# Kernel tuning notes

Hardware: AMD Instinct MI355X
Metric: run time of the kernel (lower is better)

Reference implementation:

```python
import jax, jax.numpy as jnp
import numpy as np

N = 50000   # nodes
E = 600000  # edges (avg degree 12)
D = 128     # embedding dim (hardcoded in original: np.zeros(128))
P = 5       # propagation iterations (self.p)


def setup_inputs() -> dict:
    key = jax.random.key(0)
    ks = jax.random.split(key, 10)
    x = jax.random.normal(ks[0], (N, D), jnp.float32)
    g = jax.random.normal(ks[1], (D,), jnp.float32)
    dist = jax.random.uniform(ks[2], (E,), jnp.float32)
    w1 = jax.random.normal(ks[3], (1,), jnp.float32)
    w2 = jax.random.normal(ks[4], (1,), jnp.float32)
    w3 = jax.random.normal(ks[5], (1,), jnp.float32)
    w4 = jax.random.normal(ks[6], (1,), jnp.float32)
    w5 = jax.random.normal(ks[7], (1,), jnp.float32)
    src = jax.random.randint(ks[8], (E,), 0, N)
    dst = jax.random.randint(ks[9], (E,), 0, N)
    return {"x": x, "g": g, "dist": dist, "w1": w1, "w2": w2, "w3": w3,
            "w4": w4, "w5": w5, "src": src, "dst": dst}


def reference(x, g, dist, w1, w2, w3, w4, w5, src, dst):
    # travel_times[i] = sum_{j in N(i)} w5 * dist(i,j)  -- iteration-invariant
    travel = jax.ops.segment_sum(w5[0] * dist, src, num_segments=N)  # [N]
    # per-node affine part, constant across the P iterations
    base = w1[0] * x + w2[0] * g[None, :] + w4[0] * jax.nn.relu(travel)[:, None]  # [N, D]
    u = x  # new_u_vect starts as a copy of x
    for _ in range(P):
        # u_sum[i] = sum_{j in N(i)} u[j]  (gather + segment-sum, synchronous update)
        u_sum = jax.ops.segment_sum(u[dst], src, num_segments=N)  # [N, D]
        u = base + w3[0] * u_sum
    return jax.nn.relu(u)
```

## Files before the change

kernel.cpp:

```cpp
#include <hip/hip_runtime.h>

#define D 128
#define D4 32
#define CAP 64
#define RSTRIDE 192

typedef float v4f __attribute__((ext_vector_type(4)));
typedef _Float16 h4 __attribute__((ext_vector_type(4)));

static inline size_t align_up(size_t v, size_t a) { return (v + a - 1) & ~(a - 1); }

__device__ __forceinline__ unsigned long long* rowPacked(char* rows, int n) {
  return (unsigned long long*)(rows + (size_t)n * RSTRIDE);
}
__device__ __forceinline__ const unsigned long long* rowPackedC(const char* rows, int n) {
  return (const unsigned long long*)(rows + (size_t)n * RSTRIDE);
}
__device__ __forceinline__ unsigned short* rowAdj(char* rows, int n) {
  return (unsigned short*)(rows + (size_t)n * RSTRIDE + 16);
}
__device__ __forceinline__ const unsigned short* rowAdjC(const char* rows, int n) {
  return (const unsigned short*)(rows + (size_t)n * RSTRIDE + 16);
}

__global__ void fill_ell_kernel(const int* __restrict__ src,
                                const int* __restrict__ dst,
                                const float* __restrict__ dist,
                                char* __restrict__ rows, int E) {
  int e = blockIdx.x * blockDim.x + threadIdx.x;
  if (e < E) {
    int s = src[e];
    unsigned long long fx = (unsigned long long)(dist[e] * 4294967296.0f);
    unsigned long long val = (1ull << 48) | fx;
    unsigned long long old = atomicAdd(rowPacked(rows, s), val);
    unsigned int slot = (unsigned int)(old >> 48);
    if (slot < CAP) rowAdj(rows, s)[slot] = (unsigned short)dst[e];
  }
}

__global__ void base_seed_kernel(const v4f* __restrict__ x4, const v4f* __restrict__ g4,
                                 const char* __restrict__ rows,
                                 const float* __restrict__ w1p, const float* __restrict__ w2p,
                                 const float* __restrict__ w4p, const float* __restrict__ w5p,
                                 h4* __restrict__ base, h4* __restrict__ uA,
                                 h4* __restrict__ uB, int n) {
  int i = blockIdx.x * blockDim.x + threadIdx.x;
  int node = i >> 5;
  int lane = i & 31;
  if (node > n) return;
  size_t idx = (size_t)node * 32 + lane;
  if (node == n) {
    h4 z = {0, 0, 0, 0};
    uA[idx] = z;
    uB[idx] = z;
    return;
  }
  v4f xv = x4[(size_t)node * D4 + lane];
  v4f gv = g4[lane];
  unsigned long long p = *rowPackedC(rows, node);
  float ds = (float)(p & 0xFFFFFFFFFFFFull) * (1.0f / 4294967296.0f);
  float t = w5p[0] * ds;
  t = t > 0.f ? t : 0.f;
  v4f b = w1p[0] * xv + w2p[0] * gv;
  b += t * w4p[0];
  base[idx] = __builtin_convertvector(b, h4);
  uA[idx] = __builtin_convertvector(xv, h4);
}

__global__ __launch_bounds__(256) void prop_kernel(
    const h4* __restrict__ uin, const h4* __restrict__ base,
    const char* __restrict__ rows,
    const float* __restrict__ w3p,
    void* __restrict__ uout, int n, int final_relu)
{
  int gtid = blockIdx.x * blockDim.x + threadIdx.x;
  int node = gtid >> 5;
  int lane = gtid & 31;
  if (node >= n) return;

  unsigned long long p = *rowPackedC(rows, node);
  int deg = (int)(p >> 48);
  if (deg > CAP) deg = CAP;

  const unsigned short* row = rowAdjC(rows, node);
  int a0 = row[lane];
  int a1 = row[lane + 32];

  v4f acc0 = {0.f,0.f,0.f,0.f}, acc1 = acc0, acc2 = acc0, acc3 = acc0;

  for (int k = 0; k < deg; k += 8) {
    int sel = (k >= 32) ? a1 : a0;
    int j0 = __shfl(sel, (k + 0) & 31, 32); j0 = (k + 0 < deg) ? j0 : n;
    int j1 = __shfl(sel, (k + 1) & 31, 32); j1 = (k + 1 < deg) ? j1 : n;
    int j2 = __shfl(sel, (k + 2) & 31, 32); j2 = (k + 2 < deg) ? j2 : n;
    int j3 = __shfl(sel, (k + 3) & 31, 32); j3 = (k + 3 < deg) ? j3 : n;
    int j4 = __shfl(sel, (k + 4) & 31, 32); j4 = (k + 4 < deg) ? j4 : n;
    int j5 = __shfl(sel, (k + 5) & 31, 32); j5 = (k + 5 < deg) ? j5 : n;
    int j6 = __shfl(sel, (k + 6) & 31, 32); j6 = (k + 6 < deg) ? j6 : n;
    int j7 = __shfl(sel, (k + 7) & 31, 32); j7 = (k + 7 < deg) ? j7 : n;
    h4 v0 = uin[(size_t)j0 * 32 + lane];
    h4 v1 = uin[(size_t)j1 * 32 + lane];
    h4 v2 = uin[(size_t)j2 * 32 + lane];
    h4 v3 = uin[(size_t)j3 * 32 + lane];
    h4 v4 = uin[(size_t)j4 * 32 + lane];
    h4 v5 = uin[(size_t)j5 * 32 + lane];
    h4 v6 = uin[(size_t)j6 * 32 + lane];
    h4 v7 = uin[(size_t)j7 * 32 + lane];
    acc0 += __builtin_convertvector(v0, v4f) + __builtin_convertvector(v1, v4f);
    acc1 += __builtin_convertvector(v2, v4f) + __builtin_convertvector(v3, v4f);
    acc2 += __builtin_convertvector(v4, v4f) + __builtin_convertvector(v5, v4f);
    acc3 += __builtin_convertvector(v6, v4f) + __builtin_convertvector(v7, v4f);
  }
  v4f asum = (acc0 + acc1) + (acc2 + acc3);

  size_t idx = (size_t)node * 32 + lane;
  v4f bb = __builtin_convertvector(base[idx], v4f);
  v4f r = bb + w3p[0] * asum;

  if (final_relu) {
    r.x = r.x > 0.f ? r.x : 0.f;
    r.y = r.y > 0.f ? r.y : 0.f;
    r.z = r.z > 0.f ? r.z : 0.f;
    r.w = r.w > 0.f ? r.w : 0.f;
    __builtin_nontemporal_store(r, (v4f*)uout + idx);
  } else {
    ((h4*)uout)[idx] = __builtin_convertvector(r, h4);
  }
}

extern "C" void kernel_launch(void* const* d_in, const int* in_sizes, int n_in,
                              void* d_out, int out_size, void* d_ws, size_t ws_size,
                              hipStream_t stream) {
  const float* x    = (const float*)d_in[0];
  const float* g    = (const float*)d_in[1];
  const float* dist = (const float*)d_in[2];
  const float* w1   = (const float*)d_in[3];
  const float* w2   = (const float*)d_in[4];
  const float* w3   = (const float*)d_in[5];
  const float* w4   = (const float*)d_in[6];
  const float* w5   = (const float*)d_in[7];
  const int*   src  = (const int*)d_in[8];
  const int*   dst  = (const int*)d_in[9];

  const int N = in_sizes[0] / D;
  const int E = in_sizes[2];

  char* ws = (char*)d_ws;
  size_t o = 0;
  char* rows  = ws + o;                 o += align_up((size_t)N * RSTRIDE, 256);
  h4*   baseB = (h4*)(ws + o);          o += align_up((size_t)(N + 1) * D * 2, 256);
  h4*   uA    = (h4*)(ws + o);          o += align_up((size_t)(N + 1) * D * 2, 256);
  h4*   uB    = (h4*)(ws + o);          o += align_up((size_t)(N + 1) * D * 2, 256);
  float* out  = (float*)d_out;

  hipMemsetAsync(rows, 0, (size_t)N * RSTRIDE, stream);

  const int tb = 256;
  const int eblocks = (E + tb - 1) / tb;
  const int sthreads = (N + 1) * 32;
  const int sblocks = (sthreads + tb - 1) / tb;

  fill_ell_kernel<<<eblocks, tb, 0, stream>>>(src, dst, dist, rows, E);
  base_seed_kernel<<<sblocks, tb, 0, stream>>>((const v4f*)x, (const v4f*)g, rows,
                                               w1, w2, w4, w5, baseB, uA, uB, N);

  const int pthreads = N * 32;
  const int pblocks = (pthreads + 255) / 256;
  prop_kernel<<<pblocks, 256, 0, stream>>>(uA, baseB, rows, w3, uB,  N, 0);
  prop_kernel<<<pblocks, 256, 0, stream>>>(uB, baseB, rows, w3, uA,  N, 0);
  prop_kernel<<<pblocks, 256, 0, stream>>>(uA, baseB, rows, w3, uB,  N, 0);
  prop_kernel<<<pblocks, 256, 0, stream>>>(uB, baseB, rows, w3, uA,  N, 0);
  prop_kernel<<<pblocks, 256, 0, stream>>>(uA, baseB, rows, w3, out, N, 1);
}
```

Baseline: 254.5 us.

## Split ELL adjacency into two half-edge tables with separate counters

Replaces the single interleaved per-node row (packed counter plus 64 adjacency slots in a 192-byte stride) with two separate counter arrays and two 32-slot adjacency arrays. Each half of the edge list fills its own table, which halves atomic contention per counter and shrinks the memset to only the counters. The propagation kernel walks the two halves in two loops, padding each half separately. This can add wasted padded gathers, since each half is rounded up to a multiple of 8, and it lowers per-node capacity to 32 edges per half.

```diff
diff --git a/kernel.cpp b/kernel.cpp
--- a/kernel.cpp
+++ b/kernel.cpp
@@ -2,44 +2,40 @@
 
 #define D 128
 #define D4 32
-#define CAP 64
-#define RSTRIDE 192
+#define CAPH 32
 
 typedef float v4f __attribute__((ext_vector_type(4)));
 typedef _Float16 h4 __attribute__((ext_vector_type(4)));
 
 static inline size_t align_up(size_t v, size_t a) { return (v + a - 1) & ~(a - 1); }
-
-__device__ __forceinline__ unsigned long long* rowPacked(char* rows, int n) {
-  return (unsigned long long*)(rows + (size_t)n * RSTRIDE);
-}
-__device__ __forceinline__ const unsigned long long* rowPackedC(const char* rows, int n) {
-  return (const unsigned long long*)(rows + (size_t)n * RSTRIDE);
-}
-__device__ __forceinline__ unsigned short* rowAdj(char* rows, int n) {
-  return (unsigned short*)(rows + (size_t)n * RSTRIDE + 16);
-}
-__device__ __forceinline__ const unsigned short* rowAdjC(const char* rows, int n) {
-  return (const unsigned short*)(rows + (size_t)n * RSTRIDE + 16);
-}
 
 __global__ void fill_ell_kernel(const int* __restrict__ src,
                                 const int* __restrict__ dst,
                                 const float* __restrict__ dist,
-                                char* __restrict__ rows, int E) {
+                                unsigned long long* __restrict__ packedA,
+                                unsigned long long* __restrict__ packedB,
+                                unsigned short* __restrict__ adjA,
+                                unsigned short* __restrict__ adjB,
+                                int E, int Ehalf) {
   int e = blockIdx.x * blockDim.x + threadIdx.x;
-  if (e < E) {
-    int s = src[e];
-    unsigned long long fx = (unsigned long long)(dist[e] * 4294967296.0f);
-    unsigned long long val = (1ull << 48) | fx;
-    unsigned long long old = atomicAdd(rowPacked(rows, s), val);
+  if (e >= E) return;
+  int s = src[e];
+  unsigned long long fx = (unsigned long long)(dist[e] * 4294967296.0f);
+  unsigned long long val = (1ull << 48) | fx;
+  if (e < Ehalf) {
+    unsigned long long old = atomicAdd(&packedA[s], val);
     unsigned int slot = (unsigned int)(old >> 48);
-    if (slot < CAP) rowAdj(rows, s)[slot] = (unsigned short)dst[e];
+    if (slot < CAPH) adjA[(size_t)s * CAPH + slot] = (unsigned short)dst[e];
+  } else {
+    unsigned long long old = atomicAdd(&packedB[s], val);
+    unsigned int slot = (unsigned int)(old >> 48);
+    if (slot < CAPH) adjB[(size_t)s * CAPH + slot] = (unsigned short)dst[e];
   }
 }
 
 __global__ void base_seed_kernel(const v4f* __restrict__ x4, const v4f* __restrict__ g4,
-                                 const char* __restrict__ rows,
+                                 const unsigned long long* __restrict__ packedA,
+                                 const unsigned long long* __restrict__ packedB,
                                  const float* __restrict__ w1p, const float* __restrict__ w2p,
                                  const float* __restrict__ w4p, const float* __restrict__ w5p,
                                  h4* __restrict__ base, h4* __restrict__ uA,
@@ -48,7 +44,7 @@
   int node = i >> 5;
   int lane = i & 31;
   if (node > n) return;
-  size_t idx = (size_t)node * 32 + lane;
+  size_t idx = (size_t)i;
   if (node == n) {
     h4 z = {0, 0, 0, 0};
     uA[idx] = z;
@@ -57,8 +53,9 @@
   }
   v4f xv = x4[(size_t)node * D4 + lane];
   v4f gv = g4[lane];
-  unsigned long long p = *rowPackedC(rows, node);
-  float ds = (float)(p & 0xFFFFFFFFFFFFull) * (1.0f / 4294967296.0f);
+  unsigned long long sum = (packedA[node] & 0xFFFFFFFFFFFFull)
+                         + (packedB[node] & 0xFFFFFFFFFFFFull);
+  float ds = (float)sum * (1.0f / 4294967296.0f);
   float t = w5p[0] * ds;
   t = t > 0.f ? t : 0.f;
   v4f b = w1p[0] * xv + w2p[0] * gv;
@@ -69,7 +66,10 @@
 
 __global__ __launch_bounds__(256) void prop_kernel(
     const h4* __restrict__ uin, const h4* __restrict__ base,
-    const char* __restrict__ rows,
+    const unsigned long long* __restrict__ packedA,
+    const unsigned long long* __restrict__ packedB,
+    const unsigned short* __restrict__ adjA,
+    const unsigned short* __restrict__ adjB,
     const float* __restrict__ w3p,
     void* __restrict__ uout, int n, int final_relu)
 {
@@ -78,26 +78,25 @@
   int lane = gtid & 31;
   if (node >= n) return;
 
-  unsigned long long p = *rowPackedC(rows, node);
-  int deg = (int)(p >> 48);
-  if (deg > CAP) deg = CAP;
-
-  const unsigned short* row = rowAdjC(rows, node);
-  int a0 = row[lane];
-  int a1 = row[lane + 32];
+  unsigned long long pA = packedA[node];
+  unsigned long long pB = packedB[node];
+  int degA = (int)(pA >> 48); if (degA > CAPH) degA = CAPH;
+  int degB = (int)(pB >> 48); if (degB > CAPH) degB = CAPH;
+
+  int a0 = adjA[(size_t)node * CAPH + lane];
+  int a1 = adjB[(size_t)node * CAPH + lane];
 
   v4f acc0 = {0.f,0.f,0.f,0.f}, acc1 = acc0, acc2 = acc0, acc3 = acc0;
 
-  for (int k = 0; k < deg; k += 8) {
-    int sel = (k >= 32) ? a1 : a0;
-    int j0 = __shfl(sel, (k + 0) & 31, 32); j0 = (k + 0 < deg) ? j0 : n;
-    int j1 = __shfl(sel, (k + 1) & 31, 32); j1 = (k + 1 < deg) ? j1 : n;
-    int j2 = __shfl(sel, (k + 2) & 31, 32); j2 = (k + 2 < deg) ? j2 : n;
-    int j3 = __shfl(sel, (k + 3) & 31, 32); j3 = (k + 3 < deg) ? j3 : n;
-    int j4 = __shfl(sel, (k + 4) & 31, 32); j4 = (k + 4 < deg) ? j4 : n;
-    int j5 = __shfl(sel, (k + 5) & 31, 32); j5 = (k + 5 < deg) ? j5 : n;
-    int j6 = __shfl(sel, (k + 6) & 31, 32); j6 = (k + 6 < deg) ? j6 : n;
-    int j7 = __shfl(sel, (k + 7) & 31, 32); j7 = (k + 7 < deg) ? j7 : n;
+  for (int k = 0; k < degA; k += 8) {
+    int j0 = __shfl(a0, k + 0, 32); j0 = (k + 0 < degA) ? j0 : n;
+    int j1 = __shfl(a0, k + 1, 32); j1 = (k + 1 < degA) ? j1 : n;
+    int j2 = __shfl(a0, k + 2, 32); j2 = (k + 2 < degA) ? j2 : n;
+    int j3 = __shfl(a0, k + 3, 32); j3 = (k + 3 < degA) ? j3 : n;
+    int j4 = __shfl(a0, k + 4, 32); j4 = (k + 4 < degA) ? j4 : n;
+    int j5 = __shfl(a0, k + 5, 32); j5 = (k + 5 < degA) ? j5 : n;
+    int j6 = __shfl(a0, k + 6, 32); j6 = (k + 6 < degA) ? j6 : n;
+    int j7 = __shfl(a0, k + 7, 32); j7 = (k + 7 < degA) ? j7 : n;
     h4 v0 = uin[(size_t)j0 * 32 + lane];
     h4 v1 = uin[(size_t)j1 * 32 + lane];
     h4 v2 = uin[(size_t)j2 * 32 + lane];
@@ -111,9 +110,32 @@
     acc2 += __builtin_convertvector(v4, v4f) + __builtin_convertvector(v5, v4f);
     acc3 += __builtin_convertvector(v6, v4f) + __builtin_convertvector(v7, v4f);
   }
+  for (int k = 0; k < degB; k += 8) {
+    int j0 = __shfl(a1, k + 0, 32); j0 = (k + 0 < degB) ? j0 : n;
+    int j1 = __shfl(a1, k + 1, 32); j1 = (k + 1 < degB) ? j1 : n;
+    int j2 = __shfl(a1, k + 2, 32); j2 = (k + 2 < degB) ? j2 : n;
+    int j3 = __shfl(a1, k + 3, 32); j3 = (k + 3 < degB) ? j3 : n;
+    int j4 = __shfl(a1, k + 4, 32); j4 = (k + 4 < degB) ? j4 : n;
+    int j5 = __shfl(a1, k + 5, 32); j5 = (k + 5 < degB) ? j5 : n;
+    int j6 = __shfl(a1, k + 6, 32); j6 = (k + 6 < degB) ? j6 : n;
+    int j7 = __shfl(a1, k + 7, 32); j7 = (k + 7 < degB) ? j7 : n;
+    h4 v0 = uin[(size_t)j0 * 32 + lane];
+    h4 v1 = uin[(size_t)j1 * 32 + lane];
+    h4 v2 = uin[(size_t)j2 * 32 + lane];
+    h4 v3 = uin[(size_t)j3 * 32 + lane];
+    h4 v4 = uin[(size_t)j4 * 32 + lane];
+    h4 v5 = uin[(size_t)j5 * 32 + lane];
+    h4 v6 = uin[(size_t)j6 * 32 + lane];
+    h4 v7 = uin[(size_t)j7 * 32 + lane];
+    acc0 += __builtin_convertvector(v0, v4f) + __builtin_convertvector(v1, v4f);
+    acc1 += __builtin_convertvector(v2, v4f) + __builtin_convertvector(v3, v4f);
+    acc2 += __builtin_convertvector(v4, v4f) + __builtin_convertvector(v5, v4f);
+    acc3 += __builtin_convertvector(v6, v4f) + __builtin_convertvector(v7, v4f);
+  }
   v4f asum = (acc0 + acc1) + (acc2 + acc3);
 
-  size_t idx = (size_t)node * 32 + lane;
+  size_t idx = (size_t)gtid - (size_t)0;
+  idx = (size_t)node * 32 + lane;
   v4f bb = __builtin_convertvector(base[idx], v4f);
   v4f r = bb + w3p[0] * asum;
 
@@ -144,31 +166,39 @@
 
   const int N = in_sizes[0] / D;
   const int E = in_sizes[2];
+  const int Ehalf = E / 2;
 
   char* ws = (char*)d_ws;
   size_t o = 0;
-  char* rows  = ws + o;                 o += align_up((size_t)N * RSTRIDE, 256);
-  h4*   baseB = (h4*)(ws + o);          o += align_up((size_t)(N + 1) * D * 2, 256);
-  h4*   uA    = (h4*)(ws + o);          o += align_up((size_t)(N + 1) * D * 2, 256);
-  h4*   uB    = (h4*)(ws + o);          o += align_up((size_t)(N + 1) * D * 2, 256);
-  float* out  = (float*)d_out;
-
-  hipMemsetAsync(rows, 0, (size_t)N * RSTRIDE, stream);
+  unsigned long long* packedA = (unsigned long long*)(ws + o); o += align_up((size_t)N * 8, 256);
+  unsigned long long* packedB = (unsigned long long*)(ws + o);
+  size_t zero_end = o + (size_t)N * 8;
+  o += align_up((size_t)N * 8, 256);
+  unsigned short* adjA = (unsigned short*)(ws + o); o += align_up((size_t)N * CAPH * 2, 256);
+  unsigned short* adjB = (unsigned short*)(ws + o); o += align_up((size_t)N * CAPH * 2, 256);
+  h4* baseB = (h4*)(ws + o); o += align_up((size_t)(N + 1) * D * 2, 256);
+  h4* uA    = (h4*)(ws + o); o += align_up((size_t)(N + 1) * D * 2, 256);
+  h4* uB    = (h4*)(ws + o); o += align_up((size_t)(N + 1) * D * 2, 256);
+  float* out = (float*)d_out;
+
+  hipMemsetAsync(ws, 0, zero_end, stream);
 
   const int tb = 256;
   const int eblocks = (E + tb - 1) / tb;
   const int sthreads = (N + 1) * 32;
   const int sblocks = (sthreads + tb - 1) / tb;
 
-  fill_ell_kernel<<<eblocks, tb, 0, stream>>>(src, dst, dist, rows, E);
-  base_seed_kernel<<<sblocks, tb, 0, stream>>>((const v4f*)x, (const v4f*)g, rows,
+  fill_ell_kernel<<<eblocks, tb, 0, stream>>>(src, dst, dist, packedA, packedB,
+                                              adjA, adjB, E, Ehalf);
+  base_seed_kernel<<<sblocks, tb, 0, stream>>>((const v4f*)x, (const v4f*)g,
+                                               packedA, packedB,
                                                w1, w2, w4, w5, baseB, uA, uB, N);
 
   const int pthreads = N * 32;
   const int pblocks = (pthreads + 255) / 256;
-  prop_kernel<<<pblocks, 256, 0, stream>>>(uA, baseB, rows, w3, uB,  N, 0);
-  prop_kernel<<<pblocks, 256, 0, stream>>>(uB, baseB, rows, w3, uA,  N, 0);
-  prop_kernel<<<pblocks, 256, 0, stream>>>(uA, baseB, rows, w3, uB,  N, 0);
-  prop_kernel<<<pblocks, 256, 0, stream>>>(uB, baseB, rows, w3, uA,  N, 0);
-  prop_kernel<<<pblocks, 256, 0, stream>>>(uA, baseB, rows, w3, out, N, 1);
-}
+  prop_kernel<<<pblocks, 256, 0, stream>>>(uA, baseB, packedA, packedB, adjA, adjB, w3, uB,  N, 0);
+  prop_kernel<<<pblocks, 256, 0, stream>>>(uB, baseB, packedA, packedB, adjA, adjB, w3, uA,  N, 0);
+  prop_kernel<<<pblocks, 256, 0, stream>>>(uA, baseB, packedA, packedB, adjA, adjB, w3, uB,  N, 0);
+  prop_kernel<<<pblocks, 256, 0, stream>>>(uB, baseB, packedA, packedB, adjA, adjB, w3, uA,  N, 0);
+  prop_kernel<<<pblocks, 256, 0, stream>>>(uA, baseB, packedA, packedB, adjA, adjB, w3, out, N, 1);
+}
```

After: 253.2 us. About the same (-0.5%).
